# Kernel optimization log

Measured on AMD Instinct MI355X. Metric: run time of the kernel, lower is better.

## Reference

```python
import jax, jax.numpy as jnp
import numpy as np

S = 4  # upsample scale


def setup_inputs() -> dict:
    key = jax.random.key(0)
    ks = jax.random.split(key, 8)
    B, C, H, W = 4, 128, 64, 64
    feat_lr = jax.random.normal(ks[0], (B, C, H, W), dtype=jnp.float32)
    # gate: Conv2d(C, C//4, 1, bias=False) -> LeakyReLU(0.2) -> Conv2d(C//4, 1, 1, bias=True) -> Sigmoid
    gate_w1 = jax.random.normal(ks[1], (C, C // 4), dtype=jnp.float32) * 0.05
    gate_w2 = jax.random.normal(ks[2], (C // 4, 1), dtype=jnp.float32) * 0.1
    gate_b2 = jnp.full((1,), -3.0, dtype=jnp.float32)  # init bias per module
    # mlp: Conv2d(C+2, C, 1) -> ReLU -> Conv2d(C, C, 1)
    mlp_w1 = jax.random.normal(ks[3], (C + 2, C), dtype=jnp.float32) * 0.05
    mlp_b1 = jax.random.normal(ks[4], (C,), dtype=jnp.float32) * 0.01
    mlp_w2 = jax.random.normal(ks[5], (C, C), dtype=jnp.float32) * 0.05
    mlp_b2 = jax.random.normal(ks[6], (C,), dtype=jnp.float32) * 0.01
    return {"feat_lr": feat_lr, "gate_w1": gate_w1, "gate_w2": gate_w2,
            "gate_b2": gate_b2, "mlp_w1": mlp_w1, "mlp_b1": mlp_b1,
            "mlp_w2": mlp_w2, "mlp_b2": mlp_b2}


def reference(feat_lr, gate_w1, gate_w2, gate_b2, mlp_w1, mlp_b1, mlp_w2, mlp_b2):
    B, C, H, W = feat_lr.shape
    f = jnp.transpose(feat_lr, (0, 2, 3, 1))  # (B,H,W,C)

    # ---- gate on LR grid (1x1 convs == per-pixel matmuls) ----
    g = f @ gate_w1                              # (B,H,W,C//4)
    g = jnp.where(g >= 0, g, 0.2 * g)            # LeakyReLU(0.2)
    gate = jax.nn.sigmoid(g @ gate_w2 + gate_b2) # (B,H,W,1)

    # ---- subpixel grid: channels [x, y], values in (-1,1) ----
    coords = jnp.linspace(-1.0 + 1.0 / S, 1.0 - 1.0 / S, S, dtype=feat_lr.dtype)
    yy, xx = jnp.meshgrid(coords, coords, indexing="ij")
    grid = jnp.stack([xx, yy], axis=-1)          # (S,S,2)

    # ---- mlp: split first conv weight into feat part and grid part.
    # Since convs are 1x1 and feat_hr is nearest-upsampled (constant over each
    # SxS block) while grid tiles per block, hidden = relu(f@W1f + grid@W1g + b1)
    # broadcast over (block, subpixel) — avoids materializing concat/HR inputs.
    w1_f, w1_g = mlp_w1[:C], mlp_w1[C:]          # (C,C), (2,C)
    h_f = f @ w1_f                               # (B,H,W,C)
    h_g = grid @ w1_g                            # (S,S,C)
    hidden = jax.nn.relu(h_f[:, :, None, :, None, :]
                         + h_g[None, None, :, None, :, :]
                         + mlp_b1)               # (B,H,S,W,S,C)
    res = hidden @ mlp_w2 + mlp_b2               # (B,H,S,W,S,C)

    out = res * gate[:, :, None, :, None, :]     # broadcast gate over block
    out = out.reshape(B, H * S, W * S, C)
    return jnp.transpose(out, (0, 3, 1, 2))      # (B,C,H*S,W*S)
```

## Files before the change

kernel.cpp:

```cpp
#include <hip/hip_runtime.h>
#include <hip/hip_bf16.h>
#include <math.h>


typedef __attribute__((ext_vector_type(8))) short bf16x8;
typedef __attribute__((ext_vector_type(4))) float f32x4;

__device__ inline short f2bf(float v) {
    __hip_bfloat16 b = __float2bfloat16(v);
    return *reinterpret_cast<short*>(&b);
}

__device__ inline void barrier_lgkm() {
    asm volatile("s_waitcnt lgkmcnt(0)" ::: "memory");
    __builtin_amdgcn_s_barrier();
    asm volatile("" ::: "memory");
}

__global__ __launch_bounds__(256) void ipi_pre_kernel(
    const float* __restrict__ w2,
    const float* __restrict__ w1,
    const float* __restrict__ gw1,
    __hip_bfloat16* __restrict__ w2t,
    __hip_bfloat16* __restrict__ w1t_hi,
    __hip_bfloat16* __restrict__ w1t_lo,
    __hip_bfloat16* __restrict__ g1t_hi,
    __hip_bfloat16* __restrict__ g1t_lo)
{
    int gid = blockIdx.x * 256 + threadIdx.x;
    if (gid < 16384) {
        int j = gid >> 7, k = gid & 127;
        w2t[gid] = __float2bfloat16(w2[k * 128 + j]);
    } else if (gid < 32768) {
        int i = gid - 16384, j = i >> 7, c = i & 127;
        float v = w1[c * 128 + j];
        __hip_bfloat16 hi = __float2bfloat16(v);
        w1t_hi[i] = hi;
        w1t_lo[i] = __float2bfloat16(v - __bfloat162float(hi));
    } else if (gid < 36864) {
        int i = gid - 32768, jg = i >> 7, c = i & 127;
        float v = gw1[c * 32 + jg];
        __hip_bfloat16 hi = __float2bfloat16(v);
        g1t_hi[i] = hi;
        g1t_lo[i] = __float2bfloat16(v - __bfloat162float(hi));
    }
}

__global__ __launch_bounds__(256, 4) void ipi_main(
    const float* __restrict__ feat,
    const float* __restrict__ mlp_w1,
    const float* __restrict__ mlp_b1,
    const float* __restrict__ gate_w2,
    const float* __restrict__ gate_b2,
    const float* __restrict__ mlp_b2,
    const __hip_bfloat16* __restrict__ w2t,
    const __hip_bfloat16* __restrict__ w1t_hi,
    const __hip_bfloat16* __restrict__ w1t_lo,
    const __hip_bfloat16* __restrict__ g1t_hi,
    const __hip_bfloat16* __restrict__ g1t_lo,
    float* __restrict__ out)
{
    __shared__ float hf_s[16 * 132];
    __shared__ float hgb_s[16 * 132];
    __shared__ float gate_s[16];
    __shared__ char  hid[16384];
    short* f_hi = (short*)hid;
    short* f_lo = (short*)(hid + 4352);
    float* glds = (float*)(hid + 8704);

    const int t    = threadIdx.x;
    const int lane = t & 63;
    const int lg   = lane >> 4;
    const int ml   = lane & 15;
    const int wv   = t >> 6;
    const int bx   = blockIdx.x;
    const int w0   = (bx & 3) * 16;
    const int h    = (bx >> 2) & 63;
    const int b    = bx >> 8;

    bf16x8 afrag[2][4];
    f32x4  b2v[2];
    {
        const __hip_bfloat16* base = w2t + (wv * 32 + ml) * 128 + lg * 8;
        #pragma unroll
        for (int jt = 0; jt < 2; ++jt) {
            #pragma unroll
            for (int ks = 0; ks < 4; ++ks)
                afrag[jt][ks] = *(const bf16x8*)(base + jt * 2048 + ks * 32);
            b2v[jt] = *(const f32x4*)&mlp_b2[wv * 32 + jt * 16 + lg * 4];
        }
    }

    float* ptrs[8];
    {
        float* pbase = out + ((size_t)(b * 128 + wv * 32 + lg * 4) << 16)
                           + (size_t)(h * 4) * 256 + w0 * 4 + ml;
        #pragma unroll
        for (int jt = 0; jt < 2; ++jt)
            #pragma unroll
            for (int r = 0; r < 4; ++r)
                ptrs[jt * 4 + r] = pbase + ((size_t)(jt * 16 + r) << 16);
    }

    {
        const float* fbase = feat + ((size_t)(b * 128) * 64 + h) * 64 + w0;
        #pragma unroll
        for (int i = 0; i < 8; ++i) {
            int idx = t + i * 256;
            int c = idx >> 4, w = idx & 15;
            float v = fbase[(size_t)c * 4096 + w];
            short hi = f2bf(v);
            float hf32 = __bfloat162float(*(__hip_bfloat16*)&hi);
            f_hi[w * 136 + c] = hi;
            f_lo[w * 136 + c] = f2bf(v - hf32);
        }
        #pragma unroll
        for (int i = 0; i < 8; ++i) {
            int idx = t + i * 256;
            int s = idx >> 7, k = idx & 127;
            float cx = -0.75f + 0.5f * (float)(s & 3);
            float cy = -0.75f + 0.5f * (float)(s >> 2);
            hgb_s[s * 132 + k] = cx * mlp_w1[16384 + k]
                               + cy * mlp_w1[16512 + k] + mlp_b1[k];
        }
    }
    barrier_lgkm();

    {
        bf16x8 fhi[4], flo[4];
        {
            const short* fb  = f_hi + ml * 136 + lg * 8;
            const short* flb = f_lo + ml * 136 + lg * 8;
            #pragma unroll
            for (int ks = 0; ks < 4; ++ks) {
                fhi[ks] = *(const bf16x8*)(fb + ks * 32);
                flo[ks] = *(const bf16x8*)(flb + ks * 32);
            }
        }
        #pragma unroll
        for (int jj = 0; jj < 2; ++jj) {
            const int jt16 = (wv * 2 + jj) * 16;
            const __hip_bfloat16* bh = w1t_hi + (jt16 + ml) * 128 + lg * 8;
            const __hip_bfloat16* bl = w1t_lo + (jt16 + ml) * 128 + lg * 8;
            f32x4 acc = {0.f, 0.f, 0.f, 0.f};
            #pragma unroll
            for (int ks = 0; ks < 4; ++ks) {
                bf16x8 Bh = *(const bf16x8*)(bh + ks * 32);
                bf16x8 Bl = *(const bf16x8*)(bl + ks * 32);
                acc = __builtin_amdgcn_mfma_f32_16x16x32_bf16(fhi[ks], Bh, acc, 0, 0, 0);
                acc = __builtin_amdgcn_mfma_f32_16x16x32_bf16(fhi[ks], Bl, acc, 0, 0, 0);
                acc = __builtin_amdgcn_mfma_f32_16x16x32_bf16(flo[ks], Bh, acc, 0, 0, 0);
            }
            #pragma unroll
            for (int r = 0; r < 4; ++r)
                hf_s[(lg * 4 + r) * 132 + jt16 + ml] = acc[r];
        }
        if (wv == 0) {
            #pragma unroll
            for (int jt = 0; jt < 2; ++jt) {
                const __hip_bfloat16* bh = g1t_hi + (jt * 16 + ml) * 128 + lg * 8;
                const __hip_bfloat16* bl = g1t_lo + (jt * 16 + ml) * 128 + lg * 8;
                f32x4 acc = {0.f, 0.f, 0.f, 0.f};
                #pragma unroll
                for (int ks = 0; ks < 4; ++ks) {
                    bf16x8 Bh = *(const bf16x8*)(bh + ks * 32);
                    bf16x8 Bl = *(const bf16x8*)(bl + ks * 32);
                    acc = __builtin_amdgcn_mfma_f32_16x16x32_bf16(fhi[ks], Bh, acc, 0, 0, 0);
                    acc = __builtin_amdgcn_mfma_f32_16x16x32_bf16(fhi[ks], Bl, acc, 0, 0, 0);
                    acc = __builtin_amdgcn_mfma_f32_16x16x32_bf16(flo[ks], Bh, acc, 0, 0, 0);
                }
                #pragma unroll
                for (int r = 0; r < 4; ++r) {
                    float v = acc[r];
                    glds[(lg * 4 + r) * 33 + jt * 16 + ml] = (v >= 0.f) ? v : 0.2f * v;
                }
            }
        }
    }
    barrier_lgkm();

    const int am = t & 31;
    const int ak = t >> 5;
    const int asw = (am & 7) << 4;
    auto phaseA = [&](int c) {
        const int gm = c * 32 + am;
        const float* hfr = hf_s  + ((gm >> 2) & 15) * 132 + ak * 16;
        const float* hgr = hgb_s + (((gm >> 6) << 2) | (gm & 3)) * 132 + ak * 16;
        char* wp = hid + (c & 1) * 8192 + am * 256;
        float4 a0 = *(const float4*)(hfr);
        float4 a1 = *(const float4*)(hfr + 4);
        float4 a2 = *(const float4*)(hfr + 8);
        float4 a3 = *(const float4*)(hfr + 12);
        float4 g0 = *(const float4*)(hgr);
        float4 g1 = *(const float4*)(hgr + 4);
        float4 g2 = *(const float4*)(hgr + 8);
        float4 g3 = *(const float4*)(hgr + 12);
        bf16x8 hv0, hv1;
        hv0[0] = f2bf(fmaxf(a0.x + g0.x, 0.f));
        hv0[1] = f2bf(fmaxf(a0.y + g0.y, 0.f));
        hv0[2] = f2bf(fmaxf(a0.z + g0.z, 0.f));
        hv0[3] = f2bf(fmaxf(a0.w + g0.w, 0.f));
        hv0[4] = f2bf(fmaxf(a1.x + g1.x, 0.f));
        hv0[5] = f2bf(fmaxf(a1.y + g1.y, 0.f));
        hv0[6] = f2bf(fmaxf(a1.z + g1.z, 0.f));
        hv0[7] = f2bf(fmaxf(a1.w + g1.w, 0.f));
        hv1[0] = f2bf(fmaxf(a2.x + g2.x, 0.f));
        hv1[1] = f2bf(fmaxf(a2.y + g2.y, 0.f));
        hv1[2] = f2bf(fmaxf(a2.z + g2.z, 0.f));
        hv1[3] = f2bf(fmaxf(a2.w + g2.w, 0.f));
        hv1[4] = f2bf(fmaxf(a3.x + g3.x, 0.f));
        hv1[5] = f2bf(fmaxf(a3.y + g3.y, 0.f));
        hv1[6] = f2bf(fmaxf(a3.z + g3.z, 0.f));
        hv1[7] = f2bf(fmaxf(a3.w + g3.w, 0.f));
        *(bf16x8*)(wp + ((ak * 32) ^ asw))      = hv0;
        *(bf16x8*)(wp + ((ak * 32 + 16) ^ asw)) = hv1;
    };

    if (t < 16) {
        float s = gate_b2[0];
        #pragma unroll 8
        for (int jg = 0; jg < 32; ++jg) s = fmaf(glds[t * 33 + jg], gate_w2[jg], s);
        gate_s[t] = 1.f / (1.f + expf(-s));
    }
    phaseA(0);
    barrier_lgkm();

    #pragma unroll
    for (int c = 0; c < 8; ++c) {
        if (c < 7) phaseA(c + 1);

        const char* buf = hid + (c & 1) * 8192;
        #pragma unroll
        for (int mt = 0; mt < 2; ++mt) {
            const int row = mt * 16 + ml;
            const int swb = (row & 7) << 4;
            const char* rp = buf + row * 256;
            bf16x8 bfrag[4];
            #pragma unroll
            for (int ks = 0; ks < 4; ++ks)
                bfrag[ks] = *(const bf16x8*)(rp + ((ks * 64 + lg * 16) ^ swb));

            f32x4 acc0 = b2v[0];
            f32x4 acc1 = b2v[1];
            #pragma unroll
            for (int ks = 0; ks < 4; ++ks) {
                acc0 = __builtin_amdgcn_mfma_f32_16x16x32_bf16(afrag[0][ks], bfrag[ks], acc0, 0, 0, 0);
                acc1 = __builtin_amdgcn_mfma_f32_16x16x32_bf16(afrag[1][ks], bfrag[ks], acc1, 0, 0, 0);
            }

            const float g = gate_s[((c & 1) << 3) + (row >> 2)];
            const int off = (c >> 1) * 256 + (c & 1) * 32 + mt * 16;
            #pragma unroll
            for (int r = 0; r < 4; ++r) {
                ptrs[r][off]     = acc0[r] * g;
                ptrs[4 + r][off] = acc1[r] * g;
            }
        }
        barrier_lgkm();
    }
}

extern "C" void kernel_launch(void* const* d_in, const int* in_sizes, int n_in,
                              void* d_out, int out_size, void* d_ws, size_t ws_size,
                              hipStream_t stream) {
    const float* feat = (const float*)d_in[0];
    const float* gw1  = (const float*)d_in[1];
    const float* gw2  = (const float*)d_in[2];
    const float* gb2  = (const float*)d_in[3];
    const float* w1   = (const float*)d_in[4];
    const float* b1   = (const float*)d_in[5];
    const float* w2   = (const float*)d_in[6];
    const float* b2   = (const float*)d_in[7];
    float* o = (float*)d_out;

    char* ws = (char*)d_ws;
    __hip_bfloat16* w2t    = (__hip_bfloat16*)(ws);
    __hip_bfloat16* w1t_hi = (__hip_bfloat16*)(ws + 32768);
    __hip_bfloat16* w1t_lo = (__hip_bfloat16*)(ws + 65536);
    __hip_bfloat16* g1t_hi = (__hip_bfloat16*)(ws + 98304);
    __hip_bfloat16* g1t_lo = (__hip_bfloat16*)(ws + 106496);

    ipi_pre_kernel<<<dim3(144), dim3(256), 0, stream>>>(
        w2, w1, gw1, w2t, w1t_hi, w1t_lo, g1t_hi, g1t_lo);
    ipi_main<<<dim3(1024), dim3(256), 0, stream>>>(
        feat, w1, b1, gw2, gb2, b2, w2t, w1t_hi, w1t_lo, g1t_hi, g1t_lo, o);
}
```

Before: 47.11 us.

## Halve per-block pixel tile, store hf as bf16, drop double-buffered hidden

```diff
diff --git a/kernel.cpp b/kernel.cpp
--- a/kernel.cpp
+++ b/kernel.cpp
@@ -9,6 +9,10 @@
 __device__ inline short f2bf(float v) {
     __hip_bfloat16 b = __float2bfloat16(v);
     return *reinterpret_cast<short*>(&b);
+}
+__device__ inline float bf2f(short s) {
+    __hip_bfloat16 b = *reinterpret_cast<__hip_bfloat16*>(&s);
+    return __bfloat162float(b);
 }
 
 __device__ inline void barrier_lgkm() {
@@ -46,7 +50,7 @@
     }
 }
 
-__global__ __launch_bounds__(256, 4) void ipi_main(
+__global__ __launch_bounds__(256, 5) void ipi_main(
     const float* __restrict__ feat,
     const float* __restrict__ mlp_w1,
     const float* __restrict__ mlp_b1,
@@ -60,13 +64,13 @@
     const __hip_bfloat16* __restrict__ g1t_lo,
     float* __restrict__ out)
 {
-    __shared__ float hf_s[16 * 132];
+    __shared__ short hf_s[8 * 136];
     __shared__ float hgb_s[16 * 132];
-    __shared__ float gate_s[16];
-    __shared__ char  hid[16384];
+    __shared__ float gate_s[8];
+    __shared__ float glds[8 * 33];
+    __shared__ char  hid[8192];
     short* f_hi = (short*)hid;
-    short* f_lo = (short*)(hid + 4352);
-    float* glds = (float*)(hid + 8704);
+    short* f_lo = (short*)(hid + 2176);
 
     const int t    = threadIdx.x;
     const int lane = t & 63;
@@ -74,9 +78,9 @@
     const int ml   = lane & 15;
     const int wv   = t >> 6;
     const int bx   = blockIdx.x;
-    const int w0   = (bx & 3) * 16;
-    const int h    = (bx >> 2) & 63;
-    const int b    = bx >> 8;
+    const int w0   = (bx & 7) * 8;
+    const int h    = (bx >> 3) & 63;
+    const int b    = bx >> 9;
 
     bf16x8 afrag[2][4];
     f32x4  b2v[2];
@@ -91,28 +95,19 @@
         }
     }
 
-    float* ptrs[8];
-    {
-        float* pbase = out + ((size_t)(b * 128 + wv * 32 + lg * 4) << 16)
-                           + (size_t)(h * 4) * 256 + w0 * 4 + ml;
-        #pragma unroll
-        for (int jt = 0; jt < 2; ++jt)
-            #pragma unroll
-            for (int r = 0; r < 4; ++r)
-                ptrs[jt * 4 + r] = pbase + ((size_t)(jt * 16 + r) << 16);
-    }
+    float* pb = out + ((size_t)(b * 128 + wv * 32 + lg * 4) << 16)
+                    + (size_t)(h * 4) * 256 + w0 * 4 + ml;
 
     {
         const float* fbase = feat + ((size_t)(b * 128) * 64 + h) * 64 + w0;
         #pragma unroll
-        for (int i = 0; i < 8; ++i) {
+        for (int i = 0; i < 4; ++i) {
             int idx = t + i * 256;
-            int c = idx >> 4, w = idx & 15;
+            int c = idx >> 3, w = idx & 7;
             float v = fbase[(size_t)c * 4096 + w];
             short hi = f2bf(v);
-            float hf32 = __bfloat162float(*(__hip_bfloat16*)&hi);
             f_hi[w * 136 + c] = hi;
-            f_lo[w * 136 + c] = f2bf(v - hf32);
+            f_lo[w * 136 + c] = f2bf(v - bf2f(hi));
         }
         #pragma unroll
         for (int i = 0; i < 8; ++i) {
@@ -128,13 +123,19 @@
 
     {
         bf16x8 fhi[4], flo[4];
-        {
+        if (ml < 8) {
             const short* fb  = f_hi + ml * 136 + lg * 8;
             const short* flb = f_lo + ml * 136 + lg * 8;
             #pragma unroll
             for (int ks = 0; ks < 4; ++ks) {
                 fhi[ks] = *(const bf16x8*)(fb + ks * 32);
                 flo[ks] = *(const bf16x8*)(flb + ks * 32);
+            }
+        } else {
+            #pragma unroll
+            for (int ks = 0; ks < 4; ++ks) {
+                fhi[ks] = (bf16x8)(short)0;
+                flo[ks] = (bf16x8)(short)0;
             }
         }
         #pragma unroll
@@ -151,9 +152,11 @@
                 acc = __builtin_amdgcn_mfma_f32_16x16x32_bf16(fhi[ks], Bl, acc, 0, 0, 0);
                 acc = __builtin_amdgcn_mfma_f32_16x16x32_bf16(flo[ks], Bh, acc, 0, 0, 0);
             }
-            #pragma unroll
-            for (int r = 0; r < 4; ++r)
-                hf_s[(lg * 4 + r) * 132 + jt16 + ml] = acc[r];
+            if (lg < 2) {
+                #pragma unroll
+                for (int r = 0; r < 4; ++r)
+                    hf_s[(lg * 4 + r) * 136 + jt16 + ml] = f2bf(acc[r]);
+            }
         }
         if (wv == 0) {
             #pragma unroll
@@ -169,54 +172,55 @@
                     acc = __builtin_amdgcn_mfma_f32_16x16x32_bf16(fhi[ks], Bl, acc, 0, 0, 0);
                     acc = __builtin_amdgcn_mfma_f32_16x16x32_bf16(flo[ks], Bh, acc, 0, 0, 0);
                 }
-                #pragma unroll
-                for (int r = 0; r < 4; ++r) {
-                    float v = acc[r];
-                    glds[(lg * 4 + r) * 33 + jt * 16 + ml] = (v >= 0.f) ? v : 0.2f * v;
+                if (lg < 2) {
+                    #pragma unroll
+                    for (int r = 0; r < 4; ++r) {
+                        float v = acc[r];
+                        glds[(lg * 4 + r) * 33 + jt * 16 + ml] = (v >= 0.f) ? v : 0.2f * v;
+                    }
                 }
             }
         }
     }
     barrier_lgkm();
 
-    const int am = t & 31;
-    const int ak = t >> 5;
-    const int asw = (am & 7) << 4;
-    auto phaseA = [&](int c) {
-        const int gm = c * 32 + am;
-        const float* hfr = hf_s  + ((gm >> 2) & 15) * 132 + ak * 16;
-        const float* hgr = hgb_s + (((gm >> 6) << 2) | (gm & 3)) * 132 + ak * 16;
-        char* wp = hid + (c & 1) * 8192 + am * 256;
-        float4 a0 = *(const float4*)(hfr);
-        float4 a1 = *(const float4*)(hfr + 4);
-        float4 a2 = *(const float4*)(hfr + 8);
-        float4 a3 = *(const float4*)(hfr + 12);
+    const int mq  = t >> 3;
+    const int kq  = t & 7;
+    const int aw  = mq >> 2;
+    const int asw = (mq & 7) << 4;
+    auto phaseA = [&](int q) {
+        const short* hfr = hf_s + aw * 136 + kq * 16;
+        const float* hgr = hgb_s + (q * 4 + (mq & 3)) * 132 + kq * 16;
+        char* wp = hid + mq * 256;
+        bf16x8 h0 = *(const bf16x8*)(hfr);
         float4 g0 = *(const float4*)(hgr);
         float4 g1 = *(const float4*)(hgr + 4);
+        bf16x8 hv0;
+        hv0[0] = f2bf(fmaxf(bf2f(h0[0]) + g0.x, 0.f));
+        hv0[1] = f2bf(fmaxf(bf2f(h0[1]) + g0.y, 0.f));
+        hv0[2] = f2bf(fmaxf(bf2f(h0[2]) + g0.z, 0.f));
+        hv0[3] = f2bf(fmaxf(bf2f(h0[3]) + g0.w, 0.f));
+        hv0[4] = f2bf(fmaxf(bf2f(h0[4]) + g1.x, 0.f));
+        hv0[5] = f2bf(fmaxf(bf2f(h0[5]) + g1.y, 0.f));
+        hv0[6] = f2bf(fmaxf(bf2f(h0[6]) + g1.z, 0.f));
+        hv0[7] = f2bf(fmaxf(bf2f(h0[7]) + g1.w, 0.f));
+        *(bf16x8*)(wp + ((kq * 32) ^ asw)) = hv0;
+        bf16x8 h1 = *(const bf16x8*)(hfr + 8);
         float4 g2 = *(const float4*)(hgr + 8);
         float4 g3 = *(const float4*)(hgr + 12);
-        bf16x8 hv0, hv1;
-        hv0[0] = f2bf(fmaxf(a0.x + g0.x, 0.f));
-        hv0[1] = f2bf(fmaxf(a0.y + g0.y, 0.f));
-        hv0[2] = f2bf(fmaxf(a0.z + g0.z, 0.f));
-        hv0[3] = f2bf(fmaxf(a0.w + g0.w, 0.f));
-        hv0[4] = f2bf(fmaxf(a1.x + g1.x, 0.f));
-        hv0[5] = f2bf(fmaxf(a1.y + g1.y, 0.f));
-        hv0[6] = f2bf(fmaxf(a1.z + g1.z, 0.f));
-        hv0[7] = f2bf(fmaxf(a1.w + g1.w, 0.f));
-        hv1[0] = f2bf(fmaxf(a2.x + g2.x, 0.f));
-        hv1[1] = f2bf(fmaxf(a2.y + g2.y, 0.f));
-        hv1[2] = f2bf(fmaxf(a2.z + g2.z, 0.f));
-        hv1[3] = f2bf(fmaxf(a2.w + g2.w, 0.f));
-        hv1[4] = f2bf(fmaxf(a3.x + g3.x, 0.f));
-        hv1[5] = f2bf(fmaxf(a3.y + g3.y, 0.f));
-        hv1[6] = f2bf(fmaxf(a3.z + g3.z, 0.f));
-        hv1[7] = f2bf(fmaxf(a3.w + g3.w, 0.f));
-        *(bf16x8*)(wp + ((ak * 32) ^ asw))      = hv0;
-        *(bf16x8*)(wp + ((ak * 32 + 16) ^ asw)) = hv1;
+        bf16x8 hv1;
+        hv1[0] = f2bf(fmaxf(bf2f(h1[0]) + g2.x, 0.f));
+        hv1[1] = f2bf(fmaxf(bf2f(h1[1]) + g2.y, 0.f));
+        hv1[2] = f2bf(fmaxf(bf2f(h1[2]) + g2.z, 0.f));
+        hv1[3] = f2bf(fmaxf(bf2f(h1[3]) + g2.w, 0.f));
+        hv1[4] = f2bf(fmaxf(bf2f(h1[4]) + g3.x, 0.f));
+        hv1[5] = f2bf(fmaxf(bf2f(h1[5]) + g3.y, 0.f));
+        hv1[6] = f2bf(fmaxf(bf2f(h1[6]) + g3.z, 0.f));
+        hv1[7] = f2bf(fmaxf(bf2f(h1[7]) + g3.w, 0.f));
+        *(bf16x8*)(wp + ((kq * 32 + 16) ^ asw)) = hv1;
     };
 
-    if (t < 16) {
+    if (t < 8) {
         float s = gate_b2[0];
         #pragma unroll 8
         for (int jg = 0; jg < 32; ++jg) s = fmaf(glds[t * 33 + jg], gate_w2[jg], s);
@@ -226,15 +230,12 @@
     barrier_lgkm();
 
     #pragma unroll
-    for (int c = 0; c < 8; ++c) {
-        if (c < 7) phaseA(c + 1);
-
-        const char* buf = hid + (c & 1) * 8192;
+    for (int q = 0; q < 4; ++q) {
         #pragma unroll
         for (int mt = 0; mt < 2; ++mt) {
             const int row = mt * 16 + ml;
             const int swb = (row & 7) << 4;
-            const char* rp = buf + row * 256;
+            const char* rp = hid + row * 256;
             bf16x8 bfrag[4];
             #pragma unroll
             for (int ks = 0; ks < 4; ++ks)
@@ -248,15 +249,19 @@
                 acc1 = __builtin_amdgcn_mfma_f32_16x16x32_bf16(afrag[1][ks], bfrag[ks], acc1, 0, 0, 0);
             }
 
-            const float g = gate_s[((c & 1) << 3) + (row >> 2)];
-            const int off = (c >> 1) * 256 + (c & 1) * 32 + mt * 16;
+            const float g = gate_s[row >> 2];
+            float* op = pb + q * 256 + mt * 16;
             #pragma unroll
             for (int r = 0; r < 4; ++r) {
-                ptrs[r][off]     = acc0[r] * g;
-                ptrs[4 + r][off] = acc1[r] * g;
+                op[(size_t)r << 16]        = acc0[r] * g;
+                op[(size_t)(r + 16) << 16] = acc1[r] * g;
             }
         }
         barrier_lgkm();
+        if (q < 3) {
+            phaseA(q + 1);
+            barrier_lgkm();
+        }
     }
 }
 
@@ -282,6 +287,6 @@
 
     ipi_pre_kernel<<<dim3(144), dim3(256), 0, stream>>>(
         w2, w1, gw1, w2t, w1t_hi, w1t_lo, g1t_hi, g1t_lo);
-    ipi_main<<<dim3(1024), dim3(256), 0, stream>>>(
+    ipi_main<<<dim3(2048), dim3(256), 0, stream>>>(
         feat, w1, b1, gw2, gb2, b2, w2t, w1t_hi, w1t_lo, g1t_hi, g1t_lo, o);
 }
```

Measured after the change: 63.77 us. 1.35x slower.
